# Kernel optimization log

Measured on AMD Instinct MI355X. Metric: run time of the kernel, lower is better.

## Reference

```python
import jax, jax.numpy as jnp
import numpy as np

DILATIONS = (1, 3, 5)
NUM_HEADS = 2


def _conv(x, w, b, dil=1, pad=0):
    # x: [B,C,H,W], w: [O,I,kh,kw] (OIHW), 'same'-style padding = dilation for k=3
    y = jax.lax.conv_general_dilated(
        x, w, window_strides=(1, 1), padding=[(pad, pad), (pad, pad)],
        rhs_dilation=(dil, dil), dimension_numbers=('NCHW', 'OIHW', 'NCHW'))
    return y + b[None, :, None, None]


def setup_inputs() -> dict:
    key = jax.random.key(0)
    ks = jax.random.split(key, 4)
    B, Cin, H, W = 4, 256, 64, 64
    Cout = 256
    x = jax.random.normal(ks[0], (B, Cin, H, W), dtype=jnp.float32)
    # kaiming-uniform-like init scale
    q_w = jax.random.uniform(ks[1], (Cout, Cin, 3, 3), dtype=jnp.float32,
                             minval=-1.0, maxval=1.0) * np.sqrt(6.0 / (Cin * 9))
    k_w = jax.random.uniform(ks[2], (Cout, Cin, 1, 1), dtype=jnp.float32,
                             minval=-1.0, maxval=1.0) * np.sqrt(6.0 / Cin)
    v_w = jax.random.uniform(ks[3], (Cout, Cin, 1, 1), dtype=jnp.float32,
                             minval=-1.0, maxval=1.0) * np.sqrt(6.0 / Cin)
    q_b = jnp.zeros((Cout,), jnp.float32)
    k_b = jnp.zeros((Cout,), jnp.float32)
    v_b = jnp.zeros((Cout,), jnp.float32)
    return {"x": x, "q_w": q_w, "q_b": q_b, "k_w": k_w, "k_b": k_b,
            "v_w": v_w, "v_b": v_b}


def reference(x, q_w, q_b, k_w, k_b, v_w, v_b):
    B, C, H, W = x.shape
    Cout = q_w.shape[0]
    hd = Cout // NUM_HEADS  # head_dim
    # ds_conv2d: sum of SiLU(dilated conv) over dilations 1,3,5 (padding=dilation)
    q = sum(jax.nn.silu(_conv(x, q_w, q_b, dil=d, pad=d)) for d in DILATIONS)
    k = _conv(x, k_w, k_b)
    v = _conv(x, v_w, v_b)
    N = H * W
    # [B, heads, head_dim, N]
    q = q.reshape(B, NUM_HEADS, hd, N)
    k = k.reshape(B, NUM_HEADS, hd, N)
    v = v.reshape(B, NUM_HEADS, hd, N)
    # energy[b,h,n,m] = sum_d q[b,h,d,n] * k[b,h,d,m]
    energy = jnp.einsum('bhdn,bhdm->bhnm', q, k)
    attn = jax.nn.softmax(energy / jnp.sqrt(jnp.float32(hd)), axis=-1)
    # out[b,h,n,d] = sum_m attn[b,h,n,m] * v[b,h,d,m]; then back to [B,C,H,W]
    out = jnp.einsum('bhnm,bhdm->bhdn', attn, v)
    return out.reshape(B, Cout, H, W)
```

## Files before the change

kernel.cpp:

```cpp
#include <hip/hip_runtime.h>
#include <cstdint>

typedef __attribute__((ext_vector_type(8))) _Float16 f16x8;
typedef __attribute__((ext_vector_type(4))) float f32x4;

#define DEV static __device__ __forceinline__

DEV void gld_lds16(void* lds_base, const void* gsrc) {
  __builtin_amdgcn_global_load_lds(
      (const __attribute__((address_space(1))) unsigned int*)gsrc,
      (__attribute__((address_space(3))) unsigned int*)lds_base,
      16, 0, 0);
}
DEV unsigned short f2h(float f) {
  _Float16 h = (_Float16)f;
  return __builtin_bit_cast(unsigned short, h);
}
DEV float h2f(unsigned short u) {
  _Float16 h = __builtin_bit_cast(_Float16, u);
  return (float)h;
}
DEV unsigned pk2h(float a, float b) {
  auto h2 = __builtin_amdgcn_cvt_pkrtz(a, b);
  return __builtin_bit_cast(unsigned, h2);
}
DEV float v_exp2(float x) { float r; asm("v_exp_f32 %0, %1" : "=v"(r) : "v"(x)); return r; }
DEV float v_rcp(float x) { float r; asm("v_rcp_f32 %0, %1" : "=v"(r) : "v"(x)); return r; }


__global__ __launch_bounds__(256) void k_prep_x(const float* __restrict__ x, char* __restrict__ xpad) {
  __shared__ float xs[32 * 257];
  int h = blockIdx.x, b = blockIdx.y, t = threadIdx.x;
  uint4 z = {0, 0, 0, 0};
  char* rowbase = xpad + ((size_t)(b * 74 + h + 5) * 74) * 512;
  for (int i = t; i < 320; i += 256) {
    int col = i >> 5, off = (i & 31) * 16;
    int w = (col < 5) ? col : 64 + col;
    *(uint4*)(rowbase + (size_t)w * 512 + off) = z;
  }
  if (h < 10) {
    int r = (h < 5) ? h : 64 + h;
    char* rb = xpad + ((size_t)(b * 74 + r) * 74) * 512;
    for (int i = t; i < 2368; i += 256) *(uint4*)(rb + (size_t)i * 16) = z;
  }
  const float* xb = x + (size_t)b * 1048576 + h * 64;
  for (int half = 0; half < 2; half++) {
    int w0 = half * 32;
    for (int kk = 0; kk < 32; kk++) {
      int flat = kk * 256 + t;
      int ci = flat >> 5, w = flat & 31;
      xs[w * 257 + ci] = xb[ci * 4096 + w0 + w];
    }
    __syncthreads();
    for (int g = 0; g < 4; g++) {
      int w = g * 8 + (t >> 5);
      int cg = t & 31;
      float v0 = xs[w * 257 + cg * 8 + 0], v1 = xs[w * 257 + cg * 8 + 1];
      float v2 = xs[w * 257 + cg * 8 + 2], v3 = xs[w * 257 + cg * 8 + 3];
      float v4 = xs[w * 257 + cg * 8 + 4], v5 = xs[w * 257 + cg * 8 + 5];
      float v6 = xs[w * 257 + cg * 8 + 6], v7 = xs[w * 257 + cg * 8 + 7];
      uint4 pk;
      pk.x = pk2h(v0, v1);
      pk.y = pk2h(v2, v3);
      pk.z = pk2h(v4, v5);
      pk.w = pk2h(v6, v7);
      *(uint4*)(xpad + ((size_t)((b * 74 + h + 5) * 74) + w0 + w + 5) * 512 + cg * 16) = pk;
    }
    __syncthreads();
  }
}

__global__ __launch_bounds__(256) void k_prep_w(
    const float* __restrict__ qw, const float* __restrict__ kw, const float* __restrict__ vw,
    unsigned short* __restrict__ Wq, unsigned short* __restrict__ Wk, unsigned short* __restrict__ Wv) {
  int gid = blockIdx.x * 256 + threadIdx.x;
  const float* q9 = qw + (size_t)gid * 9;
#pragma unroll
  for (int tp = 0; tp < 9; tp++) Wq[tp * 65536 + gid] = f2h(q9[tp]);
  Wk[gid] = f2h(kw[gid]);
  Wv[gid] = f2h(vw[gid]);
}

__global__ __launch_bounds__(256, 2) void k_conv_kv(
    const char* __restrict__ xpad, const unsigned short* __restrict__ Wk,
    const unsigned short* __restrict__ Wv, const float* __restrict__ kb,
    const float* __restrict__ vb, unsigned short* __restrict__ K, unsigned short* __restrict__ V) {
  __shared__ char sm[65536];
  int t = threadIdx.x, lane = t & 63, wid = t >> 6, q4 = lane >> 4, l15 = lane & 15;
  int px0 = blockIdx.x * 128;
  int b = px0 >> 12, nn = px0 & 4095;
  int h = blockIdx.y;
  int mode = blockIdx.z;
  int co0 = h * 128;
  const char* Wsrc = (const char*)(mode ? Wv : Wk);
  int wm = wid & 1, wn = wid >> 1;

#define STAGE_KV(base_, c_)                                                       \
  {                                                                               \
    for (int ch = wid * 1024; ch < 16384; ch += 4096) {                           \
      int o = ch + lane * 16;                                                     \
      int r = o >> 7;                                                             \
      int n = nn + r, hh = n >> 6, ww2 = n & 63;                                  \
      int col = (o & 127) ^ ((r & 7) << 4);                                       \
      gld_lds16((base_) + ch,                                                     \
                xpad + ((size_t)((b * 74 + hh + 5) * 74) + ww2 + 5) * 512 + (c_)*128 + col); \
    }                                                                             \
    for (int ch = wid * 1024; ch < 16384; ch += 4096) {                           \
      int o = ch + lane * 16;                                                     \
      int r = o >> 7;                                                             \
      int col = (o & 127) ^ ((r & 7) << 4);                                       \
      gld_lds16((base_) + 16384 + ch, Wsrc + (co0 + r) * 512 + (c_)*128 + col);   \
    }                                                                             \
  }

  STAGE_KV(sm, 0);
  asm volatile("s_waitcnt vmcnt(0)" ::: "memory");
  __syncthreads();

  f32x4 acc[4][4] = {};
  for (int c = 0; c < 4; c++) {
    char* cb = sm + (c & 1) * 32768;
    if (c < 3) STAGE_KV(sm + ((c & 1) ^ 1) * 32768, c + 1);
    const char* Xs = cb;
    const char* Ws = cb + 16384;
    int xg = mode ? wn : wm;
    int wg = mode ? wm : wn;
#pragma unroll
    for (int kt = 0; kt < 2; kt++) {
      f16x8 xf[4], wf[4];
#pragma unroll
      for (int i = 0; i < 4; i++) {
        int rx = xg * 64 + i * 16 + l15;
        xf[i] = *(const f16x8*)(Xs + ((rx * 128 + kt * 64 + q4 * 16) ^ ((rx & 7) << 4)));
        int rw = wg * 64 + i * 16 + l15;
        wf[i] = *(const f16x8*)(Ws + ((rw * 128 + kt * 64 + q4 * 16) ^ ((rw & 7) << 4)));
      }
#pragma unroll
      for (int m = 0; m < 4; m++)
#pragma unroll
        for (int n = 0; n < 4; n++)
          acc[m][n] = mode ? __builtin_amdgcn_mfma_f32_16x16x32_f16(wf[m], xf[n], acc[m][n], 0, 0, 0)
                           : __builtin_amdgcn_mfma_f32_16x16x32_f16(xf[m], wf[n], acc[m][n], 0, 0, 0);
    }
    asm volatile("s_waitcnt vmcnt(0)" ::: "memory");
    __syncthreads();
  }
#undef STAGE_KV
  int bh = b * 2 + h;
  if (mode == 0) {
#pragma unroll
    for (int m = 0; m < 4; m++)
#pragma unroll
      for (int n = 0; n < 4; n++) {
        int dd = wn * 64 + n * 16 + l15;
        float bias = kb[co0 + dd];
#pragma unroll
        for (int j = 0; j < 4; j++) {
          int npix = nn + wm * 64 + m * 16 + q4 * 4 + j;
          K[(size_t)(bh * 4096 + npix) * 128 + dd] = f2h(acc[m][n][j] + bias);
        }
      }
  } else {
#pragma unroll
    for (int m = 0; m < 4; m++)
#pragma unroll
      for (int j = 0; j < 4; j++) {
        int cr = wm * 64 + m * 16 + q4 * 4 + j;
        float bias = vb[co0 + cr];
#pragma unroll
        for (int n = 0; n < 4; n++) {
          int pc = nn + wn * 64 + (n >> 1) * 32 + (l15 >> 2) * 8 + (n & 1) * 4 + (l15 & 3);
          V[(size_t)(bh * 128 + cr) * 4096 + pc] = f2h(acc[m][n][j] + bias);
        }
      }
  }
}

__global__ __launch_bounds__(512, 2) void k_conv_q(
    const char* __restrict__ xpad, const unsigned short* __restrict__ Wq,
    const float* __restrict__ qb, unsigned short* __restrict__ Q) {
  extern __shared__ char sm[];
  int t = threadIdx.x, lane = t & 63, wid = t >> 6, q4 = lane >> 4, l15 = lane & 15;
  int fblk = blockIdx.x;
  int g = (fblk & 7) * 32 + (fblk >> 3);
  int h2 = g & 31, b = (g >> 5) & 3, ch2 = g >> 7;
  int h0 = h2 * 2;
  int co0 = ch2 * 128;
  int wn = wid & 1, wq = wid >> 1;
  int hr = wq >> 1, wloc = wq & 1;
  const int dil[3] = {1, 3, 5};
  const char* WqB = (const char*)Wq;
  f32x4 accd[3][2][4] = {};

#define STAGE_B(dstbuf, kh_, c_, kw_)                                             \
  {                                                                               \
    const char* src_ = WqB + (size_t)((kh_)*3 + (kw_)) * 131072 + co0 * 512 + (c_)*128; \
    char* dst_ = (dstbuf);                                                        \
    for (int ch = wid * 1024; ch < 16384; ch += 8192) {                           \
      int o = ch + lane * 16;                                                     \
      int r = o >> 7;                                                             \
      int col = (o & 127) ^ ((r & 7) << 4);                                       \
      gld_lds16(dst_ + ch, src_ + r * 512 + col);                                 \
    }                                                                             \
  }

#define STAGE_A_ROW(abase_, slot_, pr_, c_)                                       \
  {                                                                               \
    const char* src_ = xpad + ((size_t)(b * 74 + (pr_)) * 74) * 512 + (c_)*128;   \
    char* dst_ = (abase_) + (slot_)*9472;                                         \
    for (int ch = wid * 1024; ch < 9472; ch += 8192) {                            \
      int o = ch + lane * 16;                                                     \
      if (o < 9472) {                                                             \
        int r = o >> 7;                                                           \
        int col = (o & 127) ^ ((r & 7) << 4);                                     \
        gld_lds16(dst_ + ch, src_ + r * 512 + col);                               \
      }                                                                           \
    }                                                                             \
  }

#define STAGE_A(abase_, kh_, c_)                                                  \
  {                                                                               \
    if ((kh_) == 1) {                                                             \
      for (int s = 0; s < 2; s++) STAGE_A_ROW(abase_, s, h0 + s + 5, c_);         \
    } else {                                                                      \
      for (int di = 0; di < 3; di++)                                              \
        for (int s = 0; s < 2; s++)                                               \
          STAGE_A_ROW(abase_, di * 2 + s, h0 + s + ((kh_)-1) * dil[di] + 5, c_);  \
    }                                                                             \
  }

  STAGE_A(sm + 32768, 0, 0);
  STAGE_B(sm, 0, 0, 0);
  asm volatile("s_waitcnt vmcnt(0)" ::: "memory");
  __syncthreads();

  int curB = 0, curA = 0;
  for (int kh = 0; kh < 3; kh++) {
    for (int c = 0; c < 4; c++) {
      int cn2 = c + 1, khn2 = kh;
      if (cn2 == 4) { cn2 = 0; khn2 = kh + 1; }
      for (int kw = 0; kw < 3; kw++) {
        int kwn = kw + 1, cn = c, khn = kh;
        if (kwn == 3) { kwn = 0; cn = c + 1; if (cn == 4) { cn = 0; khn = kh + 1; } }
        char* Bnext = curB ? sm : sm + 16384;
        if (khn < 3) STAGE_B(Bnext, khn, cn, kwn);
        if (kw == 0 && khn2 < 3) STAGE_A(sm + 32768 + (curA ^ 1) * 56832, khn2, cn2);
        const char* Bc = curB ? sm + 16384 : sm;
        const char* Abase = sm + 32768 + curA * 56832;
        f16x8 bf[4][2];
#pragma unroll
        for (int n = 0; n < 4; n++)
#pragma unroll
          for (int kt = 0; kt < 2; kt++) {
            int rc = wn * 64 + n * 16 + l15;
            bf[n][kt] = *(const f16x8*)(Bc + ((rc * 128 + kt * 64 + q4 * 16) ^ ((rc & 7) << 4)));
          }
#pragma unroll
        for (int di = 0; di < 3; di++) {
          int dw = (kw - 1) * dil[di] + 5;
          const char* Ad = Abase + (kh == 1 ? hr : di * 2 + hr) * 9472;
          f16x8 af[2][2];
#pragma unroll
          for (int m = 0; m < 2; m++)
#pragma unroll
            for (int kt = 0; kt < 2; kt++) {
              int wp = wloc * 32 + m * 16 + l15 + dw;
              af[m][kt] = *(const f16x8*)(Ad + ((wp * 128 + kt * 64 + q4 * 16) ^ ((wp & 7) << 4)));
            }
          __builtin_amdgcn_s_setprio(1);
#pragma unroll
          for (int m = 0; m < 2; m++)
#pragma unroll
            for (int n = 0; n < 4; n++)
#pragma unroll
              for (int kt = 0; kt < 2; kt++)
                accd[di][m][n] = __builtin_amdgcn_mfma_f32_16x16x32_f16(af[m][kt], bf[n][kt], accd[di][m][n], 0, 0, 0);
          __builtin_amdgcn_s_setprio(0);
        }
        asm volatile("s_waitcnt vmcnt(0)" ::: "memory");
        __syncthreads();
        curB ^= 1;
      }
      if (khn2 < 3) curA ^= 1;
    }
  }
#undef STAGE_A
#undef STAGE_A_ROW
#undef STAGE_B
  const float LOG2E = 1.4426950408889634f;
  const float QSCALE = 0.12751879523176862f;
#pragma unroll
  for (int n = 0; n < 4; n++) {
    float bias = qb[co0 + wn * 64 + n * 16 + l15];
#pragma unroll
    for (int m = 0; m < 2; m++)
#pragma unroll
      for (int j = 0; j < 4; j++) {
        float s = 0.f;
#pragma unroll
        for (int di = 0; di < 3; di++) {
          float v = accd[di][m][n][j] + bias;
          s += v * v_rcp(1.0f + v_exp2(-v * LOG2E));
        }
        int w = wloc * 32 + m * 16 + q4 * 4 + j;
        int npix = (h0 + hr) * 64 + w;
        int dd = wn * 64 + n * 16 + l15;
        Q[((size_t)(b * 2 + ch2) * 4096 + npix) * 128 + dd] = f2h(s * QSCALE);
      }
  }
}

__global__ __launch_bounds__(256, 2) void k_attn(
    const unsigned short* __restrict__ Q, const unsigned short* __restrict__ K,
    const unsigned short* __restrict__ V, float* __restrict__ out,
    unsigned short* __restrict__ o1buf, float* __restrict__ mlbuf) {
  __shared__ char sm[65536];
  int t = threadIdx.x, lane = t & 63, wid = t >> 6, q4 = lane >> 4, l15 = lane & 15;
  int fblk = blockIdx.x;
  int g = (fblk & 7) * 64 + (fblk >> 3);
  int nb = g & 31, bh = (g >> 5) & 7, half = g >> 8;
  int b = bh >> 1, hh = bh & 1;
  int n0 = nb * 128;
  const char* Qg = (const char*)(Q + ((size_t)bh * 4096 + n0) * 128);
  const char* Kg = (const char*)(K + (size_t)bh * 4096 * 128) + half * 524288;
  const char* Vg = (const char*)(V + (size_t)bh * 128 * 4096) + half * 4096;
  f16x8 qf[2][4];
#pragma unroll
  for (int nt = 0; nt < 2; nt++)
#pragma unroll
    for (int kt = 0; kt < 4; kt++) {
      int rn = wid * 32 + nt * 16 + l15;
      qf[nt][kt] = *(const f16x8*)(Qg + (size_t)rn * 256 + kt * 64 + q4 * 16);
    }
  const char* pT0 = sm + (((l15 * 256 + 0 * 64 + q4 * 16) ^ (l15 << 4)));
  const char* pT1 = sm + (((l15 * 256 + 1 * 64 + q4 * 16) ^ (l15 << 4)));
  const char* pT2 = sm + (((l15 * 256 + 2 * 64 + q4 * 16) ^ (l15 << 4)));
  const char* pT3 = sm + (((l15 * 256 + 3 * 64 + q4 * 16) ^ (l15 << 4)));
  const char* pU0 = sm + 32768 + (((l15 * 128 + 0 * 64 + q4 * 16) ^ ((l15 & 7) << 4)));
  const char* pU1 = sm + 32768 + (((l15 * 128 + 1 * 64 + q4 * 16) ^ ((l15 & 7) << 4)));
  int ks[4], vs[4], lch[4];
#pragma unroll
  for (int c2 = 0; c2 < 4; c2++) {
    int ch = wid * 1024 + c2 * 4096;
    int o = ch + lane * 16;
    lch[c2] = ch;
    ks[c2] = o ^ (((o >> 8) & 15) << 4);
    int dd = o >> 7;
    vs[c2] = dd * 8192 + ((o & 127) ^ ((dd & 7) << 4));
  }
#pragma unroll
  for (int c2 = 0; c2 < 4; c2++) gld_lds16(sm + lch[c2], Kg + ks[c2]);
#pragma unroll
  for (int c2 = 0; c2 < 4; c2++) gld_lds16(sm + 32768 + lch[c2], Vg + vs[c2]);
  asm volatile("s_waitcnt vmcnt(0)" ::: "memory");
  __syncthreads();
  f32x4 Ofr[8][2] = {};
  float mrun[2] = {-3e38f, -3e38f};
  float lrun[2] = {0.f, 0.f};
  const char* kgp = Kg;
  const char* vgp = Vg;

#define ATTN_ITER(KB, VB, KBN, VBN, do_pf)                                          \
  {                                                                                 \
    if (do_pf) {                                                                    \
      kgp += 16384;                                                                 \
      vgp += 128;                                                                   \
      _Pragma("unroll") for (int c2 = 0; c2 < 4; c2++)                              \
          gld_lds16(sm + (KBN) + lch[c2], kgp + ks[c2]);                            \
      _Pragma("unroll") for (int c2 = 0; c2 < 4; c2++)                              \
          gld_lds16(sm + (VBN) + lch[c2], vgp + vs[c2]);                            \
    }                                                                               \
    f32x4 sT[4][2] = {};                                                            \
    _Pragma("unroll") for (int kt = 0; kt < 4; kt++) {                              \
      const char* pT = (kt == 0) ? pT0 : (kt == 1) ? pT1 : (kt == 2) ? pT2 : pT3;   \
      f16x8 kf[4];                                                                  \
      _Pragma("unroll") for (int mt = 0; mt < 4; mt++)                              \
          kf[mt] = *(const f16x8*)(pT + (KB) + mt * 4096);                          \
      __builtin_amdgcn_s_setprio(1);                                                \
      _Pragma("unroll") for (int mt = 0; mt < 4; mt++)                              \
          _Pragma("unroll") for (int nt = 0; nt < 2; nt++)                          \
              sT[mt][nt] = __builtin_amdgcn_mfma_f32_16x16x32_f16(                  \
                  kf[mt], qf[nt][kt], sT[mt][nt], 0, 0, 0);                         \
      __builtin_amdgcn_s_setprio(0);                                                \
    }                                                                               \
    unsigned U[2][4][2];                                                            \
    _Pragma("unroll") for (int nt = 0; nt < 2; nt++) {                              \
      float mx = sT[0][nt][0];                                                      \
      _Pragma("unroll") for (int mt = 0; mt < 4; mt++)                              \
          _Pragma("unroll") for (int j = 0; j < 4; j++) mx = fmaxf(mx, sT[mt][nt][j]); \
      mx = fmaxf(mx, __shfl_xor(mx, 16));                                           \
      mx = fmaxf(mx, __shfl_xor(mx, 32));                                           \
      float mn = mrun[nt];                                                          \
      if (!__all(mx - mn <= 8.f)) {                                                 \
        mn = fmaxf(mrun[nt], mx);                                                   \
        float al = v_exp2(mrun[nt] - mn);                                           \
        mrun[nt] = mn;                                                              \
        lrun[nt] *= al;                                                             \
        _Pragma("unroll") for (int dt = 0; dt < 8; dt++) Ofr[dt][nt] *= al;         \
      }                                                                             \
      float rs = 0.f;                                                               \
      _Pragma("unroll") for (int mt = 0; mt < 4; mt++) {                            \
        float p0 = v_exp2(sT[mt][nt][0] - mn);                                      \
        float p1 = v_exp2(sT[mt][nt][1] - mn);                                      \
        float p2 = v_exp2(sT[mt][nt][2] - mn);                                      \
        float p3 = v_exp2(sT[mt][nt][3] - mn);                                      \
        rs += (p0 + p1) + (p2 + p3);                                                \
        U[nt][mt][0] = pk2h(p0, p1);                                                \
        U[nt][mt][1] = pk2h(p2, p3);                                                \
      }                                                                             \
      rs += __shfl_xor(rs, 16);                                                     \
      rs += __shfl_xor(rs, 32);                                                     \
      lrun[nt] += rs;                                                               \
    }                                                                               \
    _Pragma("unroll") for (int kt = 0; kt < 2; kt++) {                              \
      const char* pU = kt ? pU1 : pU0;                                              \
      f16x8 pf[2];                                                                  \
      _Pragma("unroll") for (int nt = 0; nt < 2; nt++) {                            \
        uint4 fr;                                                                   \
        fr.x = U[nt][2 * kt][0];                                                    \
        fr.y = U[nt][2 * kt][1];                                                    \
        fr.z = U[nt][2 * kt + 1][0];                                                \
        fr.w = U[nt][2 * kt + 1][1];                                                \
        pf[nt] = __builtin_bit_cast(f16x8, fr);                                     \
      }                                                                             \
      f16x8 vf[8];                                                                  \
      _Pragma("unroll") for (int dt = 0; dt < 8; dt++)                              \
          vf[dt] = *(const f16x8*)(pU + ((VB)-32768) + dt * 2048);                  \
      __builtin_amdgcn_s_setprio(1);                                                \
      _Pragma("unroll") for (int dt = 0; dt < 8; dt++)                              \
          _Pragma("unroll") for (int nt = 0; nt < 2; nt++)                          \
              Ofr[dt][nt] = __builtin_amdgcn_mfma_f32_16x16x32_f16(                 \
                  vf[dt], pf[nt], Ofr[dt][nt], 0, 0, 0);                            \
      __builtin_amdgcn_s_setprio(0);                                                \
    }                                                                               \
    __syncthreads();                                                                \
  }

  for (int it2 = 0; it2 < 16; it2++) {
    ATTN_ITER(0, 32768, 16384, 49152, true);
    ATTN_ITER(16384, 49152, 0, 32768, (it2 < 15));
  }
#undef ATTN_ITER

  if (q4 == 0) {
#pragma unroll
    for (int nt = 0; nt < 2; nt++) {
      int n = n0 + wid * 32 + nt * 16 + l15;
      float2 ml;
      ml.x = mrun[nt];
      ml.y = lrun[nt];
      *(float2*)(mlbuf + ((size_t)(half * 8 + bh) * 4096 + n) * 2) = ml;
    }
  }
  if (half == 0) {
    float* og = out + (size_t)(b * 256 + hh * 128) * 4096 + n0 + wid * 32;
#pragma unroll
    for (int dt = 0; dt < 8; dt++)
#pragma unroll
      for (int nt = 0; nt < 2; nt++)
#pragma unroll
        for (int j = 0; j < 4; j++) {
          int dd = dt * 16 + q4 * 4 + j;
          og[(size_t)dd * 4096 + nt * 16 + l15] = Ofr[dt][nt][j];
        }
  } else {
    float li[2] = {v_rcp(lrun[0]), v_rcp(lrun[1])};
    unsigned short* og = o1buf + (size_t)bh * 128 * 4096 + n0 + wid * 32;
#pragma unroll
    for (int dt = 0; dt < 8; dt++)
#pragma unroll
      for (int nt = 0; nt < 2; nt++)
#pragma unroll
        for (int j = 0; j < 4; j++) {
          int dd = dt * 16 + q4 * 4 + j;
          og[(size_t)dd * 4096 + nt * 16 + l15] = f2h(Ofr[dt][nt][j] * li[nt]);
        }
  }
}

__global__ __launch_bounds__(256) void k_combine(
    float* __restrict__ out, const unsigned short* __restrict__ o1,
    const float* __restrict__ ml) {
  int tid = blockIdx.x * 256 + threadIdx.x;
  int n = tid & 4095, dg = (tid >> 12) & 7, bh = tid >> 15;
  float2 ml0 = *(const float2*)(ml + ((size_t)bh * 4096 + n) * 2);
  float2 ml1 = *(const float2*)(ml + ((size_t)(8 + bh) * 4096 + n) * 2);
  float ms = fmaxf(ml0.x, ml1.x);
  float a0 = v_exp2(ml0.x - ms);
  float w1 = ml1.y * v_exp2(ml1.x - ms);
  float inv = 1.f / (ml0.y * a0 + w1);
  size_t ob = ((size_t)((bh >> 1) * 256 + (bh & 1) * 128 + dg * 16)) * 4096 + n;
  size_t o1b = ((size_t)(bh * 128 + dg * 16)) * 4096 + n;
#pragma unroll 4
  for (int j = 0; j < 16; j++) {
    float v0 = out[ob + (size_t)j * 4096];
    float v1 = h2f(o1[o1b + (size_t)j * 4096]);
    out[ob + (size_t)j * 4096] = (v0 * a0 + v1 * w1) * inv;
  }
}

extern "C" void kernel_launch(void* const* d_in, const int* in_sizes, int n_in,
                              void* d_out, int out_size, void* d_ws, size_t ws_size,
                              hipStream_t stream) {
  (void)in_sizes; (void)n_in; (void)out_size;
  const float* x  = (const float*)d_in[0];
  const float* qw = (const float*)d_in[1];
  const float* qb = (const float*)d_in[2];
  const float* kw = (const float*)d_in[3];
  const float* kb = (const float*)d_in[4];
  const float* vw = (const float*)d_in[5];
  const float* vb = (const float*)d_in[6];
  char* ws = (char*)d_ws;
  if (ws_size < 37822464) return;
  char* xpad = ws;
  unsigned short* Wq = (unsigned short*)(ws + 11214848);
  unsigned short* Wk = (unsigned short*)(ws + 12394496);
  unsigned short* Wv = (unsigned short*)(ws + 12525568);
  unsigned short* Qb = (unsigned short*)(ws + 12656640);
  unsigned short* Kb = (unsigned short*)(ws + 21045248);
  unsigned short* Vb = (unsigned short*)(ws + 29433856);
  unsigned short* O1 = (unsigned short*)ws;
  float* ML = (float*)(ws + 11214848);
  k_prep_x<<<dim3(64, 4), dim3(256), 0, stream>>>(x, xpad);
  k_prep_w<<<dim3(256), dim3(256), 0, stream>>>(qw, kw, vw, Wq, Wk, Wv);
  k_conv_kv<<<dim3(128, 2, 2), dim3(256), 0, stream>>>(xpad, Wk, Wv, kb, vb, Kb, Vb);
  k_conv_q<<<dim3(256), dim3(512), 146432, stream>>>(xpad, Wq, qb, Qb);
  k_attn<<<dim3(512), dim3(256), 0, stream>>>(Qb, Kb, Vb, (float*)d_out, O1, ML);
  k_combine<<<dim3(1024), dim3(256), 0, stream>>>((float*)d_out, O1, ML);
}
```

Baseline: 166.3 us.

## Load V fragments directly from global into registers, halving attention LDS use

The attention kernel no longer stages V tiles through shared memory. Each lane loads its V MFMA fragments straight from global memory into registers after the PV product, and a partial vmcnt wait lets the K prefetch complete while the V loads stay in flight. Shared memory per block drops from 64KB to 32KB, which may allow more blocks per CU and cuts LDS traffic. The cost is more register pressure (16 extra f16x8 fragments), possibly uncoalesced 16-byte global loads with large strides, and global latency exposed if the prefetch is not far enough ahead.

```diff
diff --git a/kernel.cpp b/kernel.cpp
--- a/kernel.cpp
+++ b/kernel.cpp
@@ -314,7 +314,7 @@
     const unsigned short* __restrict__ Q, const unsigned short* __restrict__ K,
     const unsigned short* __restrict__ V, float* __restrict__ out,
     unsigned short* __restrict__ o1buf, float* __restrict__ mlbuf) {
-  __shared__ char sm[65536];
+  __shared__ char sm[32768];
   int t = threadIdx.x, lane = t & 63, wid = t >> 6, q4 = lane >> 4, l15 = lane & 15;
   int fblk = blockIdx.x;
   int g = (fblk & 7) * 64 + (fblk >> 3);
@@ -336,40 +336,38 @@
   const char* pT1 = sm + (((l15 * 256 + 1 * 64 + q4 * 16) ^ (l15 << 4)));
   const char* pT2 = sm + (((l15 * 256 + 2 * 64 + q4 * 16) ^ (l15 << 4)));
   const char* pT3 = sm + (((l15 * 256 + 3 * 64 + q4 * 16) ^ (l15 << 4)));
-  const char* pU0 = sm + 32768 + (((l15 * 128 + 0 * 64 + q4 * 16) ^ ((l15 & 7) << 4)));
-  const char* pU1 = sm + 32768 + (((l15 * 128 + 1 * 64 + q4 * 16) ^ ((l15 & 7) << 4)));
-  int ks[4], vs[4], lch[4];
+  int ks[4], lch[4];
 #pragma unroll
   for (int c2 = 0; c2 < 4; c2++) {
     int ch = wid * 1024 + c2 * 4096;
     int o = ch + lane * 16;
     lch[c2] = ch;
     ks[c2] = o ^ (((o >> 8) & 15) << 4);
-    int dd = o >> 7;
-    vs[c2] = dd * 8192 + ((o & 127) ^ ((dd & 7) << 4));
-  }
+  }
+  const char* vlp = Vg + l15 * 8192 + q4 * 16;
+  f16x8 vf[2][8];
 #pragma unroll
   for (int c2 = 0; c2 < 4; c2++) gld_lds16(sm + lch[c2], Kg + ks[c2]);
 #pragma unroll
-  for (int c2 = 0; c2 < 4; c2++) gld_lds16(sm + 32768 + lch[c2], Vg + vs[c2]);
+  for (int kt = 0; kt < 2; kt++)
+#pragma unroll
+    for (int dt = 0; dt < 8; dt++)
+      vf[kt][dt] = *(const f16x8*)(vlp + dt * 131072 + kt * 64);
   asm volatile("s_waitcnt vmcnt(0)" ::: "memory");
   __syncthreads();
   f32x4 Ofr[8][2] = {};
   float mrun[2] = {-3e38f, -3e38f};
   float lrun[2] = {0.f, 0.f};
   const char* kgp = Kg;
-  const char* vgp = Vg;
-
-#define ATTN_ITER(KB, VB, KBN, VBN, do_pf)                                          \
+
+#define ATTN_ITER(KB, KBN, do_pf)                                                   \
   {                                                                                 \
     if (do_pf) {                                                                    \
       kgp += 16384;                                                                 \
-      vgp += 128;                                                                   \
       _Pragma("unroll") for (int c2 = 0; c2 < 4; c2++)                              \
           gld_lds16(sm + (KBN) + lch[c2], kgp + ks[c2]);                            \
-      _Pragma("unroll") for (int c2 = 0; c2 < 4; c2++)                              \
-          gld_lds16(sm + (VBN) + lch[c2], vgp + vs[c2]);                            \
     }                                                                               \
+    __builtin_amdgcn_sched_barrier(0);                                              \
     f32x4 sT[4][2] = {};                                                            \
     _Pragma("unroll") for (int kt = 0; kt < 4; kt++) {                              \
       const char* pT = (kt == 0) ? pT0 : (kt == 1) ? pT1 : (kt == 2) ? pT2 : pT3;   \
@@ -413,7 +411,6 @@
       lrun[nt] += rs;                                                               \
     }                                                                               \
     _Pragma("unroll") for (int kt = 0; kt < 2; kt++) {                              \
-      const char* pU = kt ? pU1 : pU0;                                              \
       f16x8 pf[2];                                                                  \
       _Pragma("unroll") for (int nt = 0; nt < 2; nt++) {                            \
         uint4 fr;                                                                   \
@@ -423,22 +420,28 @@
         fr.w = U[nt][2 * kt + 1][1];                                                \
         pf[nt] = __builtin_bit_cast(f16x8, fr);                                     \
       }                                                                             \
-      f16x8 vf[8];                                                                  \
-      _Pragma("unroll") for (int dt = 0; dt < 8; dt++)                              \
-          vf[dt] = *(const f16x8*)(pU + ((VB)-32768) + dt * 2048);                  \
       __builtin_amdgcn_s_setprio(1);                                                \
       _Pragma("unroll") for (int dt = 0; dt < 8; dt++)                              \
           _Pragma("unroll") for (int nt = 0; nt < 2; nt++)                          \
               Ofr[dt][nt] = __builtin_amdgcn_mfma_f32_16x16x32_f16(                 \
-                  vf[dt], pf[nt], Ofr[dt][nt], 0, 0, 0);                            \
+                  vf[kt][dt], pf[nt], Ofr[dt][nt], 0, 0, 0);                        \
       __builtin_amdgcn_s_setprio(0);                                                \
     }                                                                               \
-    __syncthreads();                                                                \
+    __builtin_amdgcn_sched_barrier(0);                                              \
+    if (do_pf) {                                                                    \
+      vlp += 128;                                                                   \
+      _Pragma("unroll") for (int kt2 = 0; kt2 < 2; kt2++)                           \
+        _Pragma("unroll") for (int dt2 = 0; dt2 < 8; dt2++)                         \
+          vf[kt2][dt2] = *(const f16x8*)(vlp + dt2 * 131072 + kt2 * 64);            \
+    }                                                                               \
+    asm volatile("s_waitcnt vmcnt(16)" ::: "memory");                               \
+    __builtin_amdgcn_s_barrier();                                                   \
+    __builtin_amdgcn_sched_barrier(0);                                              \
   }
 
   for (int it2 = 0; it2 < 16; it2++) {
-    ATTN_ITER(0, 32768, 16384, 49152, true);
-    ATTN_ITER(16384, 49152, 0, 32768, (it2 < 15));
+    ATTN_ITER(0, 16384, true);
+    ATTN_ITER(16384, 0, (it2 < 15));
   }
 #undef ATTN_ITER
 
```

After: 226.8 us. +36.4%, slower.
